# Kernel tuning notes

Measured on AMD Instinct MI355X. Metric: run time of the kernel, lower is better.

## Reference

```python
import jax, jax.numpy as jnp
import numpy as np

B, D, K = 8192, 512, 4096
MAX_WORD_LENGTH = 16
RESIDUAL_THRESHOLD = 0.01
DECAY_FACTOR = 0.95
EPS_TARGET = 1e-8


def setup_inputs() -> dict:
    key = jax.random.key(0)
    k1, k2 = jax.random.split(key)
    targets = jax.random.normal(k1, (B, D), dtype=jnp.float32)
    codebook = jax.random.normal(k2, (K, D), dtype=jnp.float32)
    return {"targets": targets, "codebook": codebook}


def reference(targets, codebook):
    """Batched greedy residual pursuit (allow_negative_signs=True).

    Returns:
      seq      [B, L] int32 signed indices (>=0: add idx; <0: subtract (-idx-1)); 0 where inactive
      mask     [B, L] bool, True where a step actually emitted a symbol
      residual [B, D] final residual after pursuit
    """
    target_norm = jnp.linalg.norm(targets, axis=-1)  # [B]

    def step(residual, step_idx):
        rnorm = jnp.linalg.norm(residual, axis=-1)  # [B]
        active = (rnorm >= RESIDUAL_THRESHOLD) & (target_norm >= EPS_TARGET)
        # cosine similarity of each codebook vector with residual direction
        res_dir = residual / jnp.maximum(rnorm, 1e-12)[:, None]
        cos = jnp.einsum('bd,kd->bk', res_dir, codebook)  # [B, K]
        best = jnp.argmax(jnp.abs(cos), axis=-1)  # [B]
        best_cos = jnp.take_along_axis(cos, best[:, None], axis=-1)[:, 0]
        signed = jnp.where(best_cos >= 0, best, -(best + 1)).astype(jnp.int32)
        sign = jnp.where(best_cos >= 0, 1.0, -1.0).astype(residual.dtype)
        decay = jnp.power(jnp.asarray(DECAY_FACTOR, residual.dtype),
                          (step_idx + 1).astype(residual.dtype))
        contrib = sign[:, None] * decay * codebook[best]  # [B, D]
        new_res = jnp.where(active[:, None], residual - contrib, residual)
        out_idx = jnp.where(active, signed, 0)
        return new_res, (out_idx, active)

    residual, (seq, mask) = jax.lax.scan(step, targets, jnp.arange(MAX_WORD_LENGTH))
    return seq.T, mask.T, residual
```

## Files before the change

kernel.cpp:

```cpp
#include <hip/hip_runtime.h>
#include <hip/hip_bf16.h>

#define B_SZ 8192
#define D_SZ 512
#define K_SZ 4096
#define L_SZ 16
#define M_ALL (B_SZ + K_SZ)

typedef __attribute__((ext_vector_type(8))) short short8v;
typedef __attribute__((ext_vector_type(4))) float f32x4;
typedef _Float16 half8v __attribute__((ext_vector_type(8)));
typedef _Float16 h2 __attribute__((ext_vector_type(2)));
struct H2x4 { h2 a, b, c, d; };

typedef const __attribute__((address_space(1))) void gvoid;
typedef __attribute__((address_space(3))) void lvoid;

static __device__ __forceinline__ h2 habs2(h2 a) {
    unsigned u = __builtin_bit_cast(unsigned, a) & 0x7FFF7FFFu;
    return __builtin_bit_cast(h2, u);
}
static __device__ __forceinline__ h2 hmax2(h2 a, h2 b) {
#if __has_builtin(__builtin_elementwise_max)
    return __builtin_elementwise_max(a, b);
#else
    h2 r; r[0] = a[0] > b[0] ? a[0] : b[0]; r[1] = a[1] > b[1] ? a[1] : b[1]; return r;
#endif
}

__global__ void cast_bf16_kernel(const float* __restrict__ targets,
                                 const float* __restrict__ codebook,
                                 __hip_bfloat16* __restrict__ abf) {
    int idx = blockIdx.x * blockDim.x + threadIdx.x;
    const int total4 = (M_ALL * D_SZ) / 4;
    if (idx >= total4) return;
    int base = idx * 4;
    const float* src = (base < B_SZ * D_SZ) ? (targets + base)
                                            : (codebook + (base - B_SZ * D_SZ));
    float4 v = *(const float4*)src;
    abf[base + 0] = __float2bfloat16(v.x);
    abf[base + 1] = __float2bfloat16(v.y);
    abf[base + 2] = __float2bfloat16(v.z);
    abf[base + 3] = __float2bfloat16(v.w);
}

__global__ void cn2_kernel(const float* __restrict__ codebook,
                           double* __restrict__ cn2) {
    int row  = blockIdx.x * 4 + (threadIdx.x >> 6);
    int lane = threadIdx.x & 63;
    const float* r = codebook + (size_t)row * D_SZ;
    double s = 0.0;
#pragma unroll
    for (int j = 0; j < 8; j++) { double v = (double)r[lane + 64 * j]; s += v * v; }
#pragma unroll
    for (int o = 32; o > 0; o >>= 1) s += __shfl_down(s, o, 64);
    if (lane == 0) cn2[row] = s;
}

#define BM 128
#define BN 128
#define BK 32

__global__ __launch_bounds__(256)
void gemm_bt_kernel(const __hip_bfloat16* __restrict__ A,
                    const __hip_bfloat16* __restrict__ Bm,
                    _Float16* __restrict__ C) {
    __shared__ short As[BM * BK];
    __shared__ short Bs[BN * BK];
    const int tid  = threadIdx.x;
    const int bm   = blockIdx.y * BM;
    const int bn   = blockIdx.x * BN;
    const int wave = tid >> 6, lane = tid & 63;
    const int wm = (wave & 1) * 64, wn = (wave >> 1) * 64;
    const int row16 = lane & 15, quad = lane >> 4;
    const int koff = quad * 8;

    f32x4 acc[4][4] = {};

    const short* Ag = (const short*)A;
    const short* Bg = (const short*)Bm;
    const int srow = lane >> 2;
    const int scol = (lane & 3) * 8;

    for (int k0 = 0; k0 < D_SZ; k0 += BK) {
        __syncthreads();
#pragma unroll
        for (int c = 0; c < 2; c++) {
            int row = (wave * 2 + c) * 16 + srow;
            __builtin_amdgcn_global_load_lds(
                (gvoid*)(Ag + (size_t)(bm + row) * D_SZ + k0 + scol),
                (lvoid*)(As + row * BK + scol), 16, 0, 0);
            __builtin_amdgcn_global_load_lds(
                (gvoid*)(Bg + (size_t)(bn + row) * D_SZ + k0 + scol),
                (lvoid*)(Bs + row * BK + scol), 16, 0, 0);
        }
        __syncthreads();

        short8v af[4], bf[4];
#pragma unroll
        for (int i = 0; i < 4; i++)
            af[i] = *(const short8v*)(As + (wm + i * 16 + row16) * BK + koff);
#pragma unroll
        for (int j = 0; j < 4; j++)
            bf[j] = *(const short8v*)(Bs + (wn + j * 16 + row16) * BK + koff);
#pragma unroll
        for (int i = 0; i < 4; i++)
#pragma unroll
            for (int j = 0; j < 4; j++)
                acc[i][j] = __builtin_amdgcn_mfma_f32_16x16x32_bf16(af[i], bf[j], acc[i][j], 0, 0, 0);
    }

    if (bm < B_SZ) {
#pragma unroll
        for (int i = 0; i < 4; i++) {
            int grow = bm + wm + i * 16 + quad * 4;
#pragma unroll
            for (int j = 0; j < 4; j++) {
                int gcol = bn + wn + j * 16 + row16;
#pragma unroll
                for (int r = 0; r < 4; r++)
                    __builtin_nontemporal_store((_Float16)acc[i][j][r],
                                                &C[(size_t)(grow + r) * K_SZ + gcol]);
            }
        }
    } else {
#pragma unroll
        for (int i = 0; i < 4; i++) {
            int grow = bm + wm + i * 16 + quad * 4;
#pragma unroll
            for (int j = 0; j < 4; j++) {
                int gcol = bn + wn + j * 16 + row16;
#pragma unroll
                for (int r = 0; r < 4; r++)
                    C[(size_t)(grow + r) * K_SZ + gcol] = (_Float16)acc[i][j][r];
            }
        }
    }
}

#define MAXC 16
#define MARGIN 1.5f

__global__ __launch_bounds__(256, 4)
void pursuit_kernel(const float* __restrict__ targets,
                    const float* __restrict__ codebook,
                    const _Float16* __restrict__ S,
                    const double* __restrict__ cn2,
                    float* __restrict__ out) {
    const int wave = threadIdx.x >> 6;
    const int lane = threadIdx.x & 63;
    const int b = blockIdx.x * 4 + wave;
    const int lane8 = lane * 8;

    __shared__ alignas(16) _Float16 g_s[4][K_SZ];
    __shared__ int s_cnt[4];
    __shared__ int s_cand[4][MAXC];
    _Float16* g = g_s[wave];
    int* cnt  = &s_cnt[wave];
    int* cand = s_cand[wave];

    h2 tmax; tmax[0] = (_Float16)0; tmax[1] = (_Float16)0;
    {
        const _Float16* g0 = S + (size_t)b * K_SZ + lane8;
#pragma unroll
        for (int c = 0; c < 8; c++) {
            half8v h = __builtin_nontemporal_load((const half8v*)(g0 + c * 512));
            *(half8v*)&g[c * 512 + lane8] = h;
            H2x4 u = __builtin_bit_cast(H2x4, h);
            tmax = hmax2(tmax, hmax2(hmax2(habs2(u.a), habs2(u.b)),
                                     hmax2(habs2(u.c), habs2(u.d))));
        }
    }
    float m = fmaxf((float)tmax[0], (float)tmax[1]);

    double rres[8];
    double loc = 0.0;
    {
        const float* tg = targets + (size_t)b * D_SZ + lane8;
        f32x4 t0 = __builtin_nontemporal_load((const f32x4*)tg);
        f32x4 t1 = __builtin_nontemporal_load((const f32x4*)(tg + 4));
        rres[0] = t0[0]; rres[1] = t0[1]; rres[2] = t0[2]; rres[3] = t0[3];
        rres[4] = t1[0]; rres[5] = t1[1]; rres[6] = t1[2]; rres[7] = t1[3];
#pragma unroll
        for (int e = 0; e < 8; e++) loc += rres[e] * rres[e];
    }
#pragma unroll
    for (int o = 32; o > 0; o >>= 1) loc += __shfl_xor(loc, o, 64);
    double rn2 = loc;
    const bool tgt_ok = (sqrt(loc) >= 1e-8);

    float* out_seq  = out + (size_t)b * L_SZ;
    float* out_mask = out + (size_t)B_SZ * L_SZ + (size_t)b * L_SZ;
    float* out_res  = out + (size_t)2 * B_SZ * L_SZ + (size_t)b * D_SZ;

    double decay = 1.0;

    for (int t = 0; t < L_SZ; t++) {
        decay *= 0.95;
        bool active = (sqrt(rn2) >= 0.01) && tgt_ok;
        if (!active) {
            if (lane == 0)
                for (int tt = t; tt < L_SZ; tt++) {
                    __builtin_nontemporal_store(0.0f, &out_seq[tt]);
                    __builtin_nontemporal_store(0.0f, &out_mask[tt]);
                }
            break;
        }

        float M = m;
#pragma unroll
        for (int o = 32; o > 0; o >>= 1) M = fmaxf(M, __shfl_xor(M, o, 64));
        float thr = M - MARGIN;

        if (lane == 0) *cnt = 0;
        if (m >= thr) {
#pragma unroll
            for (int c = 0; c < 8; c++) {
                half8v h = *(const half8v*)&g[c * 512 + lane8];
#pragma unroll
                for (int e = 0; e < 8; e++) {
                    float f = fabsf((float)h[e]);
                    if (f >= thr) {
                        int q = atomicAdd(cnt, 1);
                        if (q < MAXC) cand[q] = c * 512 + lane8 + e;
                    }
                }
            }
        }
        __threadfence_block();
        int nc = min(*cnt, MAXC);

        int bk; double bv;
        float4 c0, c1;
        half8v Gh[8];
        if (nc == 1) {
            bk = __builtin_amdgcn_readfirstlane(cand[0]);
            const float* cr = codebook + (size_t)bk * D_SZ + lane8;
            const _Float16* Gp = S + (size_t)(B_SZ + bk) * K_SZ + lane8;
            c0 = *(const float4*)cr;
            c1 = *(const float4*)(cr + 4);
#pragma unroll
            for (int c = 0; c < 8; c++) Gh[c] = *(const half8v*)(Gp + c * 512);
            double s = rres[0] * (double)c0.x + rres[1] * (double)c0.y
                     + rres[2] * (double)c0.z + rres[3] * (double)c0.w
                     + rres[4] * (double)c1.x + rres[5] * (double)c1.y
                     + rres[6] * (double)c1.z + rres[7] * (double)c1.w;
#pragma unroll
            for (int o = 32; o > 0; o >>= 1) s += __shfl_xor(s, o, 64);
            bv = s;
        } else {
            bk = -1; bv = 0.0;
            for (int ci = 0; ci < nc; ci++) {
                int k = __builtin_amdgcn_readfirstlane(cand[ci]);
                const float* cr = codebook + (size_t)k * D_SZ + lane8;
                float4 d0 = *(const float4*)cr;
                float4 d1 = *(const float4*)(cr + 4);
                double s = rres[0] * (double)d0.x + rres[1] * (double)d0.y
                         + rres[2] * (double)d0.z + rres[3] * (double)d0.w
                         + rres[4] * (double)d1.x + rres[5] * (double)d1.y
                         + rres[6] * (double)d1.z + rres[7] * (double)d1.w;
#pragma unroll
                for (int o = 32; o > 0; o >>= 1) s += __shfl_xor(s, o, 64);
                if (bk < 0 || fabs(s) > fabs(bv) ||
                    (fabs(s) == fabs(bv) && k < bk)) { bk = k; bv = s; }
            }
            const float* cr = codebook + (size_t)bk * D_SZ + lane8;
            const _Float16* Gp = S + (size_t)(B_SZ + bk) * K_SZ + lane8;
            c0 = *(const float4*)cr;
            c1 = *(const float4*)(cr + 4);
#pragma unroll
            for (int c = 0; c < 8; c++) Gh[c] = *(const half8v*)(Gp + c * 512);
        }

        const double cn2bk = cn2[bk];
        double sd = ((bv >= 0.0) ? 1.0 : -1.0) * decay;
        rn2 = rn2 - 2.0 * sd * bv + sd * sd * cn2bk;
        if (lane == 0) {
            __builtin_nontemporal_store((float)((bv >= 0.0) ? bk : (-bk - 1)), &out_seq[t]);
            __builtin_nontemporal_store(1.0f, &out_mask[t]);
        }
        const float sdf = (float)sd;
        h2 sdh2; sdh2[0] = (_Float16)sdf; sdh2[1] = (_Float16)sdf;

        tmax[0] = (_Float16)0; tmax[1] = (_Float16)0;
#pragma unroll
        for (int c = 0; c < 8; c++) {
            half8v gv = *(const half8v*)&g[c * 512 + lane8];
            H2x4 ug = __builtin_bit_cast(H2x4, gv);
            H2x4 uG = __builtin_bit_cast(H2x4, Gh[c]);
            ug.a -= sdh2 * uG.a; ug.b -= sdh2 * uG.b;
            ug.c -= sdh2 * uG.c; ug.d -= sdh2 * uG.d;
            *(half8v*)&g[c * 512 + lane8] = __builtin_bit_cast(half8v, ug);
            tmax = hmax2(tmax, hmax2(hmax2(habs2(ug.a), habs2(ug.b)),
                                     hmax2(habs2(ug.c), habs2(ug.d))));
        }
        m = fmaxf((float)tmax[0], (float)tmax[1]);

        if (lane == 0) g[bk] = (_Float16)(float)(bv - sd * cn2bk);

        rres[0] -= sd * (double)c0.x; rres[1] -= sd * (double)c0.y;
        rres[2] -= sd * (double)c0.z; rres[3] -= sd * (double)c0.w;
        rres[4] -= sd * (double)c1.x; rres[5] -= sd * (double)c1.y;
        rres[6] -= sd * (double)c1.z; rres[7] -= sd * (double)c1.w;
    }

    {
        f32x4 r0, r1;
        r0[0] = (float)rres[0]; r0[1] = (float)rres[1]; r0[2] = (float)rres[2]; r0[3] = (float)rres[3];
        r1[0] = (float)rres[4]; r1[1] = (float)rres[5]; r1[2] = (float)rres[6]; r1[3] = (float)rres[7];
        __builtin_nontemporal_store(r0, (f32x4*)(out_res + lane8));
        __builtin_nontemporal_store(r1, (f32x4*)(out_res + lane8 + 4));
    }
}

extern "C" void kernel_launch(void* const* d_in, const int* in_sizes, int n_in,
                              void* d_out, int out_size, void* d_ws, size_t ws_size,
                              hipStream_t stream) {
    const float* targets  = (const float*)d_in[0];
    const float* codebook = (const float*)d_in[1];
    float* out = (float*)d_out;

    __hip_bfloat16* abf = (__hip_bfloat16*)d_ws;
    _Float16* S = (_Float16*)((char*)d_ws + (size_t)M_ALL * D_SZ * 2);
    double* cn2 = (double*)((char*)d_ws + (size_t)M_ALL * D_SZ * 2
                                        + (size_t)M_ALL * K_SZ * 2);

    int total4 = (M_ALL * D_SZ) / 4;
    cast_bf16_kernel<<<(total4 + 255) / 256, 256, 0, stream>>>(targets, codebook, abf);
    cn2_kernel<<<K_SZ / 4, 256, 0, stream>>>(codebook, cn2);

    dim3 ggrid(K_SZ / BN, M_ALL / BM);
    gemm_bt_kernel<<<ggrid, 256, 0, stream>>>(abf, abf + (size_t)B_SZ * D_SZ, S);

    pursuit_kernel<<<B_SZ / 4, 256, 0, stream>>>(targets, codebook, S, cn2, out);
}
```

Before: 335.4 us.

## Swizzle GEMM workgroup order, vectorize fp16 output stores, shrink pursuit blocks

The GEMM now remaps workgroup IDs with an XCD-style swizzle so neighbouring tiles land on the same chiplet's L2. It also swaps the MFMA operand order so each lane holds four consecutive columns, which lets it write 8-byte half4 vectors instead of scalar fp16 stores. The pursuit kernel switches from four waves per block to two, halving its LDS use per block so more blocks can be resident. This trades larger store transactions and better cache locality against a changed mapping that must still cover every tile exactly once.

```diff
diff --git a/kernel.cpp b/kernel.cpp
--- a/kernel.cpp
+++ b/kernel.cpp
@@ -10,6 +10,7 @@
 typedef __attribute__((ext_vector_type(8))) short short8v;
 typedef __attribute__((ext_vector_type(4))) float f32x4;
 typedef _Float16 half8v __attribute__((ext_vector_type(8)));
+typedef _Float16 half4v __attribute__((ext_vector_type(4)));
 typedef _Float16 h2 __attribute__((ext_vector_type(2)));
 struct H2x4 { h2 a, b, c, d; };
 
@@ -60,6 +61,8 @@
 #define BM 128
 #define BN 128
 #define BK 32
+#define GRID_X (K_SZ / BN)
+#define NWG ((M_ALL / BM) * GRID_X)
 
 __global__ __launch_bounds__(256)
 void gemm_bt_kernel(const __hip_bfloat16* __restrict__ A,
@@ -68,8 +71,12 @@
     __shared__ short As[BM * BK];
     __shared__ short Bs[BN * BK];
     const int tid  = threadIdx.x;
-    const int bm   = blockIdx.y * BM;
-    const int bn   = blockIdx.x * BN;
+
+    int flat = blockIdx.y * GRID_X + blockIdx.x;
+    int swz  = (flat & 7) * (NWG / 8) + (flat >> 3);
+    const int bm = (swz >> 5) * BM;
+    const int bn = (swz & 31) * BN;
+
     const int wave = tid >> 6, lane = tid & 63;
     const int wm = (wave & 1) * 64, wn = (wave >> 1) * 64;
     const int row16 = lane & 15, quad = lane >> 4;
@@ -107,32 +114,33 @@
         for (int i = 0; i < 4; i++)
 #pragma unroll
             for (int j = 0; j < 4; j++)
-                acc[i][j] = __builtin_amdgcn_mfma_f32_16x16x32_bf16(af[i], bf[j], acc[i][j], 0, 0, 0);
-    }
-
+                acc[i][j] = __builtin_amdgcn_mfma_f32_16x16x32_bf16(bf[j], af[i], acc[i][j], 0, 0, 0);
+    }
+
+    const int grow0 = bm + wm + row16;
+    const int gcol0 = bn + wn + quad * 4;
     if (bm < B_SZ) {
 #pragma unroll
         for (int i = 0; i < 4; i++) {
-            int grow = bm + wm + i * 16 + quad * 4;
+            size_t rbase = (size_t)(grow0 + i * 16) * K_SZ;
 #pragma unroll
             for (int j = 0; j < 4; j++) {
-                int gcol = bn + wn + j * 16 + row16;
-#pragma unroll
-                for (int r = 0; r < 4; r++)
-                    __builtin_nontemporal_store((_Float16)acc[i][j][r],
-                                                &C[(size_t)(grow + r) * K_SZ + gcol]);
+                half4v p;
+                p[0] = (_Float16)acc[i][j][0]; p[1] = (_Float16)acc[i][j][1];
+                p[2] = (_Float16)acc[i][j][2]; p[3] = (_Float16)acc[i][j][3];
+                __builtin_nontemporal_store(p, (half4v*)&C[rbase + gcol0 + j * 16]);
             }
         }
     } else {
 #pragma unroll
         for (int i = 0; i < 4; i++) {
-            int grow = bm + wm + i * 16 + quad * 4;
+            size_t rbase = (size_t)(grow0 + i * 16) * K_SZ;
 #pragma unroll
             for (int j = 0; j < 4; j++) {
-                int gcol = bn + wn + j * 16 + row16;
-#pragma unroll
-                for (int r = 0; r < 4; r++)
-                    C[(size_t)(grow + r) * K_SZ + gcol] = (_Float16)acc[i][j][r];
+                half4v p;
+                p[0] = (_Float16)acc[i][j][0]; p[1] = (_Float16)acc[i][j][1];
+                p[2] = (_Float16)acc[i][j][2]; p[3] = (_Float16)acc[i][j][3];
+                *(half4v*)&C[rbase + gcol0 + j * 16] = p;
             }
         }
     }
@@ -141,7 +149,7 @@
 #define MAXC 16
 #define MARGIN 1.5f
 
-__global__ __launch_bounds__(256, 4)
+__global__ __launch_bounds__(128, 4)
 void pursuit_kernel(const float* __restrict__ targets,
                     const float* __restrict__ codebook,
                     const _Float16* __restrict__ S,
@@ -149,12 +157,12 @@
                     float* __restrict__ out) {
     const int wave = threadIdx.x >> 6;
     const int lane = threadIdx.x & 63;
-    const int b = blockIdx.x * 4 + wave;
+    const int b = blockIdx.x * 2 + wave;
     const int lane8 = lane * 8;
 
-    __shared__ alignas(16) _Float16 g_s[4][K_SZ];
-    __shared__ int s_cnt[4];
-    __shared__ int s_cand[4][MAXC];
+    __shared__ alignas(16) _Float16 g_s[2][K_SZ];
+    __shared__ int s_cnt[2];
+    __shared__ int s_cand[2][MAXC];
     _Float16* g = g_s[wave];
     int* cnt  = &s_cnt[wave];
     int* cand = s_cand[wave];
@@ -329,8 +337,8 @@
     cast_bf16_kernel<<<(total4 + 255) / 256, 256, 0, stream>>>(targets, codebook, abf);
     cn2_kernel<<<K_SZ / 4, 256, 0, stream>>>(codebook, cn2);
 
-    dim3 ggrid(K_SZ / BN, M_ALL / BM);
+    dim3 ggrid(GRID_X, M_ALL / BM);
     gemm_bt_kernel<<<ggrid, 256, 0, stream>>>(abf, abf + (size_t)B_SZ * D_SZ, S);
 
-    pursuit_kernel<<<B_SZ / 4, 256, 0, stream>>>(targets, codebook, S, cn2, out);
-}
+    pursuit_kernel<<<B_SZ / 2, 128, 0, stream>>>(targets, codebook, S, cn2, out);
+}
```

Measured after the change: 367.0 us. +9.4%, slower.
